# Performance work log

Measured on AMD Instinct MI355X. Metric: run time of the kernel, lower is better.

Reference implementation:

```python
import jax, jax.numpy as jnp
import numpy as np

B, S, T, H, E = 256, 512, 16, 1024, 512  # batch, src_len, trg_steps, hidden, emb_dim


def setup_inputs() -> dict:
    key = jax.random.key(0)
    ks = jax.random.split(key, 10)
    rn = lambda k, sh: jax.random.normal(k, sh, dtype=jnp.float32) * 0.05
    return {
        "trg_emb": rn(ks[0], (B, T, E)),
        "h0": rn(ks[1], (B, H)),
        "c0": rn(ks[2], (B, H)),
        "ctx": rn(ks[3], (B, S, H)),
        "src_len": jax.random.randint(ks[4], (B,), 1, S + 1, dtype=jnp.int32),
        "W_ih": rn(ks[5], (4 * H, E + H)),  # input-feeding: lstm in = emb + hidden
        "W_hh": rn(ks[6], (4 * H, H)),
        "b_ih": jnp.zeros((4 * H,), jnp.float32),
        "b_hh": jnp.zeros((4 * H,), jnp.float32),
        "W_in": rn(ks[7], (H, H)),    # attention linear_in (no bias)
        "W_out": rn(ks[8], (H, 2 * H)),  # attention linear_out (no bias)
    }


def reference(trg_emb, h0, c0, ctx, src_len, W_ih, W_hh, b_ih, b_hh, W_in, W_out):
    # mask[b, s] = s < src_len[b]
    mask = jnp.arange(S)[None, :] < src_len[:, None]  # (B, S)
    neg = jnp.float32(-1e9)

    def step(carry, emb_t):
        h, c, h_tilde = carry  # each (B, H); emb_t (B, E)
        # input feeding: concat target embedding with previous attentional vector
        x = jnp.concatenate([emb_t, h_tilde], axis=1)  # (B, E+H)
        gates = x @ W_ih.T + b_ih + h @ W_hh.T + b_hh  # (B, 4H), pytorch gate order i,f,g,o
        i, f, g, o = jnp.split(gates, 4, axis=1)
        i = jax.nn.sigmoid(i); f = jax.nn.sigmoid(f)
        g = jnp.tanh(g);       o = jax.nn.sigmoid(o)
        c = f * c + i * g
        h = o * jnp.tanh(c)
        # Luong soft-dot attention with src_len masking
        target = h @ W_in.T                                # (B, H)
        scores = jnp.einsum('bsh,bh->bs', ctx, target)     # (B, S)
        scores = jnp.where(mask, scores, neg)
        attn = jax.nn.softmax(scores, axis=-1)
        weighted = jnp.einsum('bs,bsh->bh', attn, ctx)     # (B, H)
        h_tilde = jnp.tanh(jnp.concatenate([weighted, h], axis=1) @ W_out.T)
        return (h, c, h_tilde), h_tilde

    # initial h_tilde = init_hidden[0] (per the original code)
    (h_f, c_f, _), hs = jax.lax.scan(step, (h0, c0, h0), jnp.swapaxes(trg_emb, 0, 1))
    output = jnp.swapaxes(hs, 0, 1)  # (B, T, H)
    return output, h_f, c_f
```

## Files before the change

kernel.cpp:

```cpp
#include <hip/hip_runtime.h>
#include <cstdint>
#include <cstddef>


#define B_ 256
#define S_ 512
#define T_ 16
#define H_ 1024
#define E_ 512
#define NBUF 6

typedef unsigned short u16;
using short8 = __attribute__((ext_vector_type(8))) short;
using f32x4  = __attribute__((ext_vector_type(4))) float;

__device__ __forceinline__ float bf2f(u16 u) {
  union { uint32_t i; float f; } v; v.i = ((uint32_t)u) << 16; return v.f;
}
__device__ __forceinline__ u16 f2bf(float f) {
  union { uint32_t i; float f; } v; v.f = f;
  uint32_t r = v.i + 0x7fffu + ((v.i >> 16) & 1u);
  return (u16)(r >> 16);
}
__device__ __forceinline__ ushort4 cvt4bf(float4 v) {
  ushort4 o; o.x = f2bf(v.x); o.y = f2bf(v.y); o.z = f2bf(v.z); o.w = f2bf(v.w);
  return o;
}
__device__ __forceinline__ float sigmoidf_(float x) { return 1.f / (1.f + __expf(-x)); }

__device__ __forceinline__ void gload_lds16(const void* g, void* l) {
  __builtin_amdgcn_global_load_lds(
      (const __attribute__((address_space(1))) void*)g,
      (__attribute__((address_space(3))) void*)l, 16, 0, 0);
}

struct Reg3 { const u16* A; int lda; const u16* B; int ldb; int kt; };

template <int EPI>
__global__ __launch_bounds__(256) void gemm_k(Reg3 r0, Reg3 r1, Reg3 r2,
                                              int nmb,
                                              float* __restrict__ Cf,
                                              u16* __restrict__ Cb,
                                              const float* __restrict__ bsum,
                                              float* __restrict__ cst,
                                              u16* __restrict__ hbfo,
                                              float* __restrict__ outHC,
                                              const int tstep) {
  __shared__ u16 smA[NBUF][4096];
  __shared__ u16 smB[NBUF][4096];
  const int tid = threadIdx.x;
  const int lane = tid & 63;
  const int wave = tid >> 6;
  const int wm = wave >> 1, wn = wave & 1;
  const int m0 = (blockIdx.x % nmb) * 64;
  const int n0 = (blockIdx.x / nmb) * 64;
  const int row16 = lane & 15;
  const int kg = lane >> 4;
  const int nt = r0.kt + r1.kt + r2.kt;

  auto stage = [&](int ti, int buf) {
    const int k01 = r0.kt + r1.kt;
    const u16* Ap = (ti < r0.kt) ? r0.A : (ti < k01) ? r1.A : r2.A;
    const u16* Bp = (ti < r0.kt) ? r0.B : (ti < k01) ? r1.B : r2.B;
    const int lda = (ti < r0.kt) ? r0.lda : (ti < k01) ? r1.lda : r2.lda;
    const int ldb = (ti < r0.kt) ? r0.ldb : (ti < k01) ? r1.ldb : r2.ldb;
    const int base = (ti < r0.kt) ? 0 : (ti < k01) ? r0.kt : k01;
    const int kr = (ti - base) << 6;
#pragma unroll
    for (int j = 0; j < 2; ++j) {
      const int c = j * 256 + tid;
      const int row = c >> 3, q = c & 7;
      gload_lds16(Ap + (size_t)(m0 + row) * lda + kr + ((q ^ (row & 7)) << 3),
                  (char*)&smA[buf][0] + (size_t)(j * 256 + wave * 64) * 16);
    }
#pragma unroll
    for (int j = 0; j < 2; ++j) {
      const int c = j * 256 + tid;
      const int row = c >> 3, q = c & 7;
      gload_lds16(Bp + (size_t)(n0 + row) * ldb + kr + ((q ^ (row & 7)) << 3),
                  (char*)&smB[buf][0] + (size_t)(j * 256 + wave * 64) * 16);
    }
  };

  f32x4 acc[2][2] = {};
  stage(0, 0);
  if (nt > 1) stage(1, 1);
  if (nt > 2) stage(2, 2);
  if (nt > 3) stage(3, 3);
  for (int ti = 0; ti < nt; ++ti) {
    const int buf = ti % NBUF;
    if (ti + 4 < nt) {
      stage(ti + 4, (ti + 4) % NBUF);
      asm volatile("s_waitcnt vmcnt(16)" ::: "memory");
    } else if (ti + 3 < nt) {
      asm volatile("s_waitcnt vmcnt(12)" ::: "memory");
    } else if (ti + 2 < nt) {
      asm volatile("s_waitcnt vmcnt(8)" ::: "memory");
    } else if (ti + 1 < nt) {
      asm volatile("s_waitcnt vmcnt(4)" ::: "memory");
    } else {
      asm volatile("s_waitcnt vmcnt(0)" ::: "memory");
    }
    __builtin_amdgcn_s_barrier();
    __builtin_amdgcn_sched_barrier(0);
#pragma unroll
    for (int ks = 0; ks < 2; ++ks) {
      short8 af[2], bfr[2];
#pragma unroll
      for (int mi = 0; mi < 2; ++mi) {
        const int R = wm * 32 + mi * 16 + row16;
        af[mi] = *(const short8*)((const char*)&smA[buf][0] +
                                  (size_t)(((R << 3) | ((ks * 4 + kg) ^ (R & 7))) << 4));
      }
#pragma unroll
      for (int ni = 0; ni < 2; ++ni) {
        const int R = wn * 32 + ni * 16 + row16;
        bfr[ni] = *(const short8*)((const char*)&smB[buf][0] +
                                   (size_t)(((R << 3) | ((ks * 4 + kg) ^ (R & 7))) << 4));
      }
      asm volatile("s_waitcnt lgkmcnt(0)" ::: "memory");
      __builtin_amdgcn_sched_barrier(0);
#pragma unroll
      for (int mi = 0; mi < 2; ++mi)
#pragma unroll
        for (int ni = 0; ni < 2; ++ni)
          acc[mi][ni] = __builtin_amdgcn_mfma_f32_16x16x32_bf16(af[mi], bfr[ni], acc[mi][ni], 0, 0, 0);
      __builtin_amdgcn_sched_barrier(0);
    }
  }
#pragma unroll
  for (int mi = 0; mi < 2; ++mi) {
#pragma unroll
    for (int ni = 0; ni < 2; ++ni) {
#pragma unroll
      for (int r = 0; r < 4; ++r) {
        const int row = m0 + wm * 32 + mi * 16 + (kg << 2) + r;
        const int col = n0 + wn * 32 + ni * 16 + row16;
        float v = acc[mi][ni][r];
        if (EPI == 1) {
          Cb[row * H_ + col] = f2bf(v);
        } else if (EPI == 2) {
          float tv = tanhf(v);
          Cf[(size_t)row * (T_ * H_) + (size_t)tstep * H_ + col] = tv;
          Cb[row * H_ + col] = f2bf(tv);
        } else {
          v += bsum[col];
          float v1 = __shfl_xor(v, 1);
          float v2 = __shfl_xor(v, 2);
          float v3 = __shfl_xor(v, 3);
          if ((lane & 3) == 0) {
            const int u = col >> 2;
            float iv = sigmoidf_(v);
            float fv = sigmoidf_(v1);
            float gv = tanhf(v2);
            float ov = sigmoidf_(v3);
            float cn = fv * cst[row * H_ + u] + iv * gv;
            float hn = ov * tanhf(cn);
            cst[row * H_ + u] = cn;
            hbfo[row * H_ + u] = f2bf(hn);
            if (outHC) {
              outHC[row * H_ + u] = hn;
              outHC[B_ * H_ + row * H_ + u] = cn;
            }
          }
        }
      }
    }
  }
}

__device__ __forceinline__ int fidx(int lane, int j) {
  return (j << 6) + ((lane + (j << 2)) & 63);
}

__global__ __launch_bounds__(512, 4) void attn_pair(const u16* __restrict__ tgt,
                                                    const u16* __restrict__ ctxc,
                                                    const int* __restrict__ woffs,
                                                    const int* __restrict__ src_len,
                                                    u16* __restrict__ wwbf,
                                                    float* __restrict__ pacc,
                                                    float* __restrict__ pml,
                                                    int* __restrict__ flag) {
  __shared__ float facc[7][1024];
  __shared__ float fm[8], fl[8];
  const int p = blockIdx.x >> 1;
  const int half = blockIdx.x & 1;
  const int tid = threadIdx.x;
  const int lane = tid & 63;
  const int wave = tid >> 6;
  const int len = src_len[p];
  const int len2 = (len + 1) >> 1;
  const u16* cb = ctxc + ((size_t)woffs[p] << 10);

  float tg[16];
  {
    const u16* tp = tgt + p * H_ + lane * 16;
    short8 v1 = *(const short8*)tp;
    short8 v2 = *(const short8*)(tp + 8);
#pragma unroll
    for (int j = 0; j < 8; ++j) { tg[j] = bf2f((u16)v1[j]); tg[8 + j] = bf2f((u16)v2[j]); }
  }
  float m = -1e30f, l = 0.f;
  float acc[16];
#pragma unroll
  for (int j = 0; j < 16; ++j) acc[j] = 0.f;

  auto process = [&](int s) {
    const u16* cr = cb + ((size_t)s << 10) + (lane << 4);
    short8 v1 = *(const short8*)cr;
    short8 v2 = *(const short8*)(cr + 8);
    float cf[16];
#pragma unroll
    for (int j = 0; j < 8; ++j) { cf[j] = bf2f((u16)v1[j]); cf[8 + j] = bf2f((u16)v2[j]); }
    float x = 0.f;
#pragma unroll
    for (int j = 0; j < 16; ++j) x += cf[j] * tg[j];
#pragma unroll
    for (int off = 1; off < 64; off <<= 1) x += __shfl_xor(x, off);
    if (x > m) {
      float sc_ = __expf(m - x);
      l *= sc_;
#pragma unroll
      for (int j = 0; j < 16; ++j) acc[j] *= sc_;
      m = x;
    }
    float pv = __expf(x - m);
    l += pv;
#pragma unroll
    for (int j = 0; j < 16; ++j) acc[j] += pv * cf[j];
  };

  const int lo = half ? len2 : 0;
  const int hi = half ? len : len2;
  for (int s = lo + wave; s < hi; s += 8) process(s);

  if (wave >= 1) {
#pragma unroll
    for (int j = 0; j < 16; ++j) facc[wave - 1][fidx(lane, j)] = acc[j];
    if (lane == 0) { fm[wave] = m; fl[wave] = l; }
  }
  __syncthreads();
  if (wave == 0) {
#pragma unroll
    for (int w = 1; w < 8; ++w) {
      float pm2 = fm[w], pl2 = fl[w];
      float M = fmaxf(m, pm2);
      float e1 = __expf(m - M), e2 = __expf(pm2 - M);
#pragma unroll
      for (int j = 0; j < 16; ++j)
        acc[j] = acc[j] * e1 + facc[w - 1][fidx(lane, j)] * e2;
      l = l * e1 + pl2 * e2;
      m = M;
    }
    if (half == 1) {
      float* pa = pacc + (size_t)p * 1024;
#pragma unroll
      for (int j4 = 0; j4 < 4; ++j4) {
        float4 v;
        v.x = acc[j4 * 4]; v.y = acc[j4 * 4 + 1];
        v.z = acc[j4 * 4 + 2]; v.w = acc[j4 * 4 + 3];
        *(float4*)&pa[lane * 16 + j4 * 4] = v;
      }
      if (lane == 0) { pml[2 * p] = m; pml[2 * p + 1] = l; }
      asm volatile("s_waitcnt vmcnt(0)" ::: "memory");
      if (lane == 0)
        __hip_atomic_store(flag + p, 1, __ATOMIC_RELEASE, __HIP_MEMORY_SCOPE_AGENT);
    } else {
      int got = 0;
      if (lane == 0) {
        for (unsigned c2 = 0; c2 < (1u << 10); ++c2) {
          if (__hip_atomic_load(flag + p, __ATOMIC_RELAXED, __HIP_MEMORY_SCOPE_AGENT) != 0) {
            got = 1; break;
          }
          __builtin_amdgcn_s_sleep(2);
        }
        if (got)
          (void)__hip_atomic_load(flag + p, __ATOMIC_ACQUIRE, __HIP_MEMORY_SCOPE_AGENT);
      }
      got = __shfl(got, 0);
      if (got) {
        const float* pa = pacc + (size_t)p * 1024;
        float pm2 = pml[2 * p], pl2 = pml[2 * p + 1];
        float M = fmaxf(m, pm2);
        float e1 = __expf(m - M), e2 = __expf(pm2 - M);
#pragma unroll
        for (int j = 0; j < 16; ++j)
          acc[j] = acc[j] * e1 + pa[lane * 16 + j] * e2;
        l = l * e1 + pl2 * e2;
        m = M;
      } else {
        for (int s = len2; s < len; ++s) process(s);
      }
      const float inv = 1.f / l;
#pragma unroll
      for (int j4 = 0; j4 < 4; ++j4) {
        ushort4 o;
        o.x = f2bf(acc[j4 * 4] * inv);
        o.y = f2bf(acc[j4 * 4 + 1] * inv);
        o.z = f2bf(acc[j4 * 4 + 2] * inv);
        o.w = f2bf(acc[j4 * 4 + 3] * inv);
        *(ushort4*)(wwbf + p * H_ + lane * 16 + j4 * 4) = o;
      }
    }
  }
}

__global__ __launch_bounds__(256) void convert_all(
    const float* __restrict__ W_ih, const float* __restrict__ W_hh,
    const float* __restrict__ W_in, const float* __restrict__ W_out,
    const float* __restrict__ trg_emb, const float* __restrict__ ctx,
    const float* __restrict__ b_ih, const float* __restrict__ b_hh,
    const float* __restrict__ h0, const float* __restrict__ c0,
    const int* __restrict__ src_len,
    u16* __restrict__ wWih, u16* __restrict__ wWhh, u16* __restrict__ wWin,
    u16* __restrict__ wWout, u16* __restrict__ wemb,
    float* __restrict__ wbsum, u16* __restrict__ wh0, u16* __restrict__ whtbf,
    float* __restrict__ wc, int* __restrict__ woffs, u16* __restrict__ ctxc) {
  __shared__ int tmp[256];
  const int bid = blockIdx.x;
  const int tid = threadIdx.x;
  const int gtid = bid * 256 + tid;
  const int GSZ = 1024 * 256;
  for (int i = gtid; i < 1572864; i += GSZ) {
    const int r = i / 384, c4 = i - r * 384;
    const int rp = ((r & 1023) << 2) + (r >> 10);
    ((ushort4*)wWih)[(size_t)rp * 384 + c4] = cvt4bf(((const float4*)W_ih)[i]);
  }
  for (int i = gtid; i < 1048576; i += GSZ) {
    const int r = i >> 8, c4 = i & 255;
    const int rp = ((r & 1023) << 2) + (r >> 10);
    ((ushort4*)wWhh)[(size_t)rp * 256 + c4] = cvt4bf(((const float4*)W_hh)[i]);
  }
  for (int i = gtid; i < 262144; i += GSZ)
    ((ushort4*)wWin)[i] = cvt4bf(((const float4*)W_in)[i]);
  for (int i = gtid; i < 524288; i += GSZ)
    ((ushort4*)wWout)[i] = cvt4bf(((const float4*)W_out)[i]);
  for (int i = gtid; i < 524288; i += GSZ)
    ((ushort4*)wemb)[i] = cvt4bf(((const float4*)trg_emb)[i]);
  if (gtid < 4096) {
    const int cp = ((gtid & 1023) << 2) + (gtid >> 10);
    wbsum[cp] = b_ih[gtid] + b_hh[gtid];
  }
  for (int i = gtid; i < 262144; i += GSZ) {
    u16 hb = f2bf(h0[i]);
    wh0[i] = hb;
    whtbf[i] = hb;
    wc[i] = c0[i];
  }
  if (bid >= 768) {
    const int b = bid - 768;
    tmp[tid] = (tid < b) ? src_len[tid] : 0;
    __syncthreads();
    for (int o = 128; o > 0; o >>= 1) {
      if (tid < o) tmp[tid] += tmp[tid + o];
      __syncthreads();
    }
    const int off = tmp[0];
    if (tid == 0) woffs[b] = off;
    const int n4 = src_len[b] << 8;
    const float4* s = (const float4*)(ctx + ((size_t)b << 19));
    ushort4* d = (ushort4*)(ctxc + ((size_t)off << 10));
    for (int i = tid; i < n4; i += 256) d[i] = cvt4bf(s[i]);
  }
}

extern "C" void kernel_launch(void* const* d_in, const int* in_sizes, int n_in,
                              void* d_out, int out_size, void* d_ws, size_t ws_size,
                              hipStream_t stream) {
  const float* trg_emb = (const float*)d_in[0];
  const float* h0      = (const float*)d_in[1];
  const float* c0      = (const float*)d_in[2];
  const float* ctx     = (const float*)d_in[3];
  const int*   src_len = (const int*)d_in[4];
  const float* W_ih    = (const float*)d_in[5];
  const float* W_hh    = (const float*)d_in[6];
  const float* b_ih    = (const float*)d_in[7];
  const float* b_hh    = (const float*)d_in[8];
  const float* W_in    = (const float*)d_in[9];
  const float* W_out   = (const float*)d_in[10];
  float* out = (float*)d_out;

  char* w = (char*)d_ws;
  size_t off = 0;
  auto alloc = [&](size_t bytes) { char* p = w + off; off += bytes; return p; };
  u16*   wWih  = (u16*)  alloc(12582912);
  u16*   wWhh  = (u16*)  alloc(8388608);
  u16*   wWin  = (u16*)  alloc(2097152);
  u16*   wWout = (u16*)  alloc(4194304);
  u16*   wemb  = (u16*)  alloc(4194304);
  float* wbsum = (float*)alloc(16384);
  float* wc    = (float*)alloc(1048576);
  u16*   wh0   = (u16*)  alloc(524288);
  u16*   wh1   = (u16*)  alloc(524288);
  u16*   whtbf = (u16*)  alloc(524288);
  u16*   wtgt  = (u16*)  alloc(524288);
  u16*   wwbf  = (u16*)  alloc(524288);
  int*   woffs = (int*)  alloc(1024);
  int*   wflag = (int*)  alloc(16384);
  float* pacc  = (float*)alloc(1048576);
  float* pml   = (float*)alloc(2048);
  u16*   wctxc = (u16*)  alloc(268435456);
  (void)ws_size;

  hipMemsetAsync(wflag, 0, 16384, stream);
  convert_all<<<dim3(1024), dim3(256), 0, stream>>>(
      W_ih, W_hh, W_in, W_out, trg_emb, ctx, b_ih, b_hh, h0, c0, src_len,
      wWih, wWhh, wWin, wWout, wemb, wbsum, wh0, whtbf, wc, woffs, wctxc);

  Reg3 rz = { nullptr, 0, nullptr, 0, 0 };
  for (int t = 0; t < T_; ++t) {
    const u16* hcur = (t & 1) ? wh1 : wh0;
    u16* hnxt = (t & 1) ? wh0 : wh1;
    Reg3 g0 = { wemb + (size_t)t * E_, T_ * E_, wWih,      E_ + H_, 8 };
    Reg3 g1 = { whtbf,                 H_,      wWih + E_, E_ + H_, 16 };
    Reg3 g2 = { hcur,                  H_,      wWhh,      H_,      16 };
    gemm_k<3><<<dim3(256), dim3(256), 0, stream>>>(
        g0, g1, g2, 4, nullptr, nullptr, wbsum, wc, hnxt,
        (t == T_ - 1) ? out + (size_t)B_ * T_ * H_ : nullptr, 0);
    Reg3 i0 = { hnxt, H_, wWin, H_, 16 };
    gemm_k<1><<<dim3(64), dim3(256), 0, stream>>>(
        i0, rz, rz, 4, nullptr, wtgt, nullptr, nullptr, nullptr, nullptr, 0);
    attn_pair<<<dim3(512), dim3(512), 0, stream>>>(
        wtgt, wctxc, woffs, src_len, wwbf, pacc, pml, wflag + t * 256);
    Reg3 o0 = { wwbf, H_, wWout,      2 * H_, 16 };
    Reg3 o1 = { hnxt, H_, wWout + H_, 2 * H_, 16 };
    gemm_k<2><<<dim3(64), dim3(256), 0, stream>>>(
        o0, o1, rz, 4, out, whtbf, nullptr, nullptr, nullptr, nullptr, t);
  }
}
```

Measured before the change: 1.914 ms.

## Fuse attention linear_in GEMM into attention kernel with flag-based handoff and length ordering

```diff
diff --git a/kernel.cpp b/kernel.cpp
--- a/kernel.cpp
+++ b/kernel.cpp
@@ -32,6 +32,10 @@
   __builtin_amdgcn_global_load_lds(
       (const __attribute__((address_space(1))) void*)g,
       (__attribute__((address_space(3))) void*)l, 16, 0, 0);
+}
+
+__device__ __forceinline__ void st_flag(int* p) {
+  __hip_atomic_store(p, 1, __ATOMIC_RELEASE, __HIP_MEMORY_SCOPE_AGENT);
 }
 
 struct Reg3 { const u16* A; int lda; const u16* B; int ldb; int kt; };
@@ -137,9 +141,7 @@
         const int row = m0 + wm * 32 + mi * 16 + (kg << 2) + r;
         const int col = n0 + wn * 32 + ni * 16 + row16;
         float v = acc[mi][ni][r];
-        if (EPI == 1) {
-          Cb[row * H_ + col] = f2bf(v);
-        } else if (EPI == 2) {
+        if (EPI == 2) {
           float tv = tanhf(v);
           Cf[(size_t)row * (T_ * H_) + (size_t)tstep * H_ + col] = tv;
           Cb[row * H_ + col] = f2bf(tv);
@@ -173,33 +175,165 @@
   return (j << 6) + ((lane + (j << 2)) & 63);
 }
 
-__global__ __launch_bounds__(512, 4) void attn_pair(const u16* __restrict__ tgt,
-                                                    const u16* __restrict__ ctxc,
-                                                    const int* __restrict__ woffs,
-                                                    const int* __restrict__ src_len,
-                                                    u16* __restrict__ wwbf,
-                                                    float* __restrict__ pacc,
-                                                    float* __restrict__ pml,
-                                                    int* __restrict__ flag) {
-  __shared__ float facc[7][1024];
-  __shared__ float fm[8], fl[8];
-  const int p = blockIdx.x >> 1;
-  const int half = blockIdx.x & 1;
+struct AP {
+  const u16* hrow;
+  const u16* Win;
+  u16* tgt;
+  const u16* ctxc;
+  const int* woffs;
+  const int* src_len;
+  const int* worder;
+  u16* wwbf;
+  float* pacc;
+  float* pml;
+  int* tflag;
+  int* pflag;
+};
+
+union SMemF {
+  struct { u16 A[4][4096]; u16 B[4][4096]; } g;
+  struct { float facc[7][1024]; float fm[8]; float fl[8];
+           float tgtf[1024]; int ok; } a;
+};
+
+__global__ __launch_bounds__(512, 4) void attn_fused(AP P) {
+  __shared__ SMemF sm;
   const int tid = threadIdx.x;
+  const int bid = blockIdx.x;
   const int lane = tid & 63;
   const int wave = tid >> 6;
-  const int len = src_len[p];
+
+  if (bid < 64) {
+    const int m0 = (bid & 3) * 64;
+    const int n0 = (bid >> 2) * 64;
+    if (tid < 256) {
+      const int wv = tid >> 6;
+      const int wm = wv >> 1, wn = wv & 1;
+      const int row16 = lane & 15, kg = lane >> 4;
+      auto stage = [&](int ti, int buf) {
+        const int kr = ti << 6;
+#pragma unroll
+        for (int j = 0; j < 2; ++j) {
+          const int c = j * 256 + tid;
+          const int r = c >> 3, q = c & 7;
+          gload_lds16(P.hrow + (size_t)(m0 + r) * H_ + kr + ((q ^ (r & 7)) << 3),
+                      (char*)&sm.g.A[buf][0] + (size_t)(j * 256 + wv * 64) * 16);
+        }
+#pragma unroll
+        for (int j = 0; j < 2; ++j) {
+          const int c = j * 256 + tid;
+          const int r = c >> 3, q = c & 7;
+          gload_lds16(P.Win + (size_t)(n0 + r) * H_ + kr + ((q ^ (r & 7)) << 3),
+                      (char*)&sm.g.B[buf][0] + (size_t)(j * 256 + wv * 64) * 16);
+        }
+      };
+      f32x4 acc[2][2] = {};
+      stage(0, 0);
+      stage(1, 1);
+      for (int ti = 0; ti < 16; ++ti) {
+        const int buf = ti & 3;
+        if (ti + 2 < 16) {
+          stage(ti + 2, (ti + 2) & 3);
+          asm volatile("s_waitcnt vmcnt(8)" ::: "memory");
+        } else if (ti + 1 < 16) {
+          asm volatile("s_waitcnt vmcnt(4)" ::: "memory");
+        } else {
+          asm volatile("s_waitcnt vmcnt(0)" ::: "memory");
+        }
+        __builtin_amdgcn_s_barrier();
+        __builtin_amdgcn_sched_barrier(0);
+#pragma unroll
+        for (int ks = 0; ks < 2; ++ks) {
+          short8 af[2], bfr[2];
+#pragma unroll
+          for (int mi = 0; mi < 2; ++mi) {
+            const int R = wm * 32 + mi * 16 + row16;
+            af[mi] = *(const short8*)((const char*)&sm.g.A[buf][0] +
+                                      (size_t)(((R << 3) | ((ks * 4 + kg) ^ (R & 7))) << 4));
+          }
+#pragma unroll
+          for (int ni = 0; ni < 2; ++ni) {
+            const int R = wn * 32 + ni * 16 + row16;
+            bfr[ni] = *(const short8*)((const char*)&sm.g.B[buf][0] +
+                                       (size_t)(((R << 3) | ((ks * 4 + kg) ^ (R & 7))) << 4));
+          }
+          asm volatile("s_waitcnt lgkmcnt(0)" ::: "memory");
+          __builtin_amdgcn_sched_barrier(0);
+#pragma unroll
+          for (int mi = 0; mi < 2; ++mi)
+#pragma unroll
+            for (int ni = 0; ni < 2; ++ni)
+              acc[mi][ni] = __builtin_amdgcn_mfma_f32_16x16x32_bf16(af[mi], bfr[ni], acc[mi][ni], 0, 0, 0);
+          __builtin_amdgcn_sched_barrier(0);
+        }
+      }
+#pragma unroll
+      for (int mi = 0; mi < 2; ++mi)
+#pragma unroll
+        for (int ni = 0; ni < 2; ++ni)
+#pragma unroll
+          for (int r = 0; r < 4; ++r) {
+            const int row = m0 + wm * 32 + mi * 16 + (kg << 2) + r;
+            const int col = n0 + wn * 32 + ni * 16 + row16;
+            P.tgt[row * H_ + col] = f2bf(acc[mi][ni][r]);
+          }
+    } else {
+      for (int i = 0; i < 16; ++i) __builtin_amdgcn_s_barrier();
+    }
+    __syncthreads();
+    if (tid == 0) st_flag(P.tflag + (bid & 3) * 16 + (bid >> 2));
+  }
+
+  const int p = bid >> 1;
+  const int half = bid & 1;
+  const int row = P.worder[p];
+  const int len = P.src_len[row];
   const int len2 = (len + 1) >> 1;
-  const u16* cb = ctxc + ((size_t)woffs[p] << 10);
+  const u16* cb = P.ctxc + ((size_t)P.woffs[row] << 10);
+  const int mt = row >> 6;
+
+  {
+    int got = 1;
+    if (wave == 0) {
+      if (lane < 16) {
+        int* tf = P.tflag + mt * 16 + lane;
+        unsigned c = 0;
+        while (__hip_atomic_load(tf, __ATOMIC_RELAXED, __HIP_MEMORY_SCOPE_AGENT) == 0 &&
+               c < (1u << 16)) {
+          __builtin_amdgcn_s_sleep(4);
+          ++c;
+        }
+        got = (__hip_atomic_load(tf, __ATOMIC_ACQUIRE, __HIP_MEMORY_SCOPE_AGENT) != 0) ? 1 : 0;
+      }
+      unsigned long long mk = __ballot(got != 0);
+      if (lane == 0) sm.a.ok = ((mk & 0xFFFFull) == 0xFFFFull) ? 1 : 0;
+    }
+    __syncthreads();
+  }
+  const int allok = sm.a.ok;
+  if (!allok) {
+    const u16* hr = P.hrow + (size_t)row * H_;
+    for (int j = tid; j < H_; j += 512) {
+      float a = 0.f;
+      const u16* wr = P.Win + (size_t)j * H_;
+      for (int k = 0; k < H_; ++k) a += bf2f(hr[k]) * bf2f(wr[k]);
+      sm.a.tgtf[j] = bf2f(f2bf(a));
+    }
+    __syncthreads();
+  }
 
   float tg[16];
-  {
-    const u16* tp = tgt + p * H_ + lane * 16;
+  if (allok) {
+    const u16* tp = P.tgt + row * H_ + lane * 16;
     short8 v1 = *(const short8*)tp;
     short8 v2 = *(const short8*)(tp + 8);
 #pragma unroll
     for (int j = 0; j < 8; ++j) { tg[j] = bf2f((u16)v1[j]); tg[8 + j] = bf2f((u16)v2[j]); }
-  }
+  } else {
+#pragma unroll
+    for (int j = 0; j < 16; ++j) tg[j] = sm.a.tgtf[lane * 16 + j];
+  }
+
   float m = -1e30f, l = 0.f;
   float acc[16];
 #pragma unroll
@@ -234,26 +368,27 @@
   const int hi = half ? len : len2;
   for (int s = lo + wave; s < hi; s += 8) process(s);
 
+  __syncthreads();
   if (wave >= 1) {
 #pragma unroll
-    for (int j = 0; j < 16; ++j) facc[wave - 1][fidx(lane, j)] = acc[j];
-    if (lane == 0) { fm[wave] = m; fl[wave] = l; }
+    for (int j = 0; j < 16; ++j) sm.a.facc[wave - 1][fidx(lane, j)] = acc[j];
+    if (lane == 0) { sm.a.fm[wave] = m; sm.a.fl[wave] = l; }
   }
   __syncthreads();
   if (wave == 0) {
 #pragma unroll
     for (int w = 1; w < 8; ++w) {
-      float pm2 = fm[w], pl2 = fl[w];
+      float pm2 = sm.a.fm[w], pl2 = sm.a.fl[w];
       float M = fmaxf(m, pm2);
       float e1 = __expf(m - M), e2 = __expf(pm2 - M);
 #pragma unroll
       for (int j = 0; j < 16; ++j)
-        acc[j] = acc[j] * e1 + facc[w - 1][fidx(lane, j)] * e2;
+        acc[j] = acc[j] * e1 + sm.a.facc[w - 1][fidx(lane, j)] * e2;
       l = l * e1 + pl2 * e2;
       m = M;
     }
     if (half == 1) {
-      float* pa = pacc + (size_t)p * 1024;
+      float* pa = P.pacc + (size_t)p * 1024;
 #pragma unroll
       for (int j4 = 0; j4 < 4; ++j4) {
         float4 v;
@@ -261,26 +396,25 @@
         v.z = acc[j4 * 4 + 2]; v.w = acc[j4 * 4 + 3];
         *(float4*)&pa[lane * 16 + j4 * 4] = v;
       }
-      if (lane == 0) { pml[2 * p] = m; pml[2 * p + 1] = l; }
+      if (lane == 0) { P.pml[2 * p] = m; P.pml[2 * p + 1] = l; }
       asm volatile("s_waitcnt vmcnt(0)" ::: "memory");
-      if (lane == 0)
-        __hip_atomic_store(flag + p, 1, __ATOMIC_RELEASE, __HIP_MEMORY_SCOPE_AGENT);
+      if (lane == 0) st_flag(P.pflag + p);
     } else {
       int got = 0;
       if (lane == 0) {
         for (unsigned c2 = 0; c2 < (1u << 10); ++c2) {
-          if (__hip_atomic_load(flag + p, __ATOMIC_RELAXED, __HIP_MEMORY_SCOPE_AGENT) != 0) {
+          if (__hip_atomic_load(P.pflag + p, __ATOMIC_RELAXED, __HIP_MEMORY_SCOPE_AGENT) != 0) {
             got = 1; break;
           }
           __builtin_amdgcn_s_sleep(2);
         }
         if (got)
-          (void)__hip_atomic_load(flag + p, __ATOMIC_ACQUIRE, __HIP_MEMORY_SCOPE_AGENT);
+          (void)__hip_atomic_load(P.pflag + p, __ATOMIC_ACQUIRE, __HIP_MEMORY_SCOPE_AGENT);
       }
       got = __shfl(got, 0);
       if (got) {
-        const float* pa = pacc + (size_t)p * 1024;
-        float pm2 = pml[2 * p], pl2 = pml[2 * p + 1];
+        const float* pa = P.pacc + (size_t)p * 1024;
+        float pm2 = P.pml[2 * p], pl2 = P.pml[2 * p + 1];
         float M = fmaxf(m, pm2);
         float e1 = __expf(m - M), e2 = __expf(pm2 - M);
 #pragma unroll
@@ -299,7 +433,7 @@
         o.y = f2bf(acc[j4 * 4 + 1] * inv);
         o.z = f2bf(acc[j4 * 4 + 2] * inv);
         o.w = f2bf(acc[j4 * 4 + 3] * inv);
-        *(ushort4*)(wwbf + p * H_ + lane * 16 + j4 * 4) = o;
+        *(ushort4*)(P.wwbf + row * H_ + lane * 16 + j4 * 4) = o;
       }
     }
   }
@@ -315,8 +449,10 @@
     u16* __restrict__ wWih, u16* __restrict__ wWhh, u16* __restrict__ wWin,
     u16* __restrict__ wWout, u16* __restrict__ wemb,
     float* __restrict__ wbsum, u16* __restrict__ wh0, u16* __restrict__ whtbf,
-    float* __restrict__ wc, int* __restrict__ woffs, u16* __restrict__ ctxc) {
+    float* __restrict__ wc, int* __restrict__ woffs, u16* __restrict__ ctxc,
+    int* __restrict__ worder) {
   __shared__ int tmp[256];
+  __shared__ int skey[256];
   const int bid = blockIdx.x;
   const int tid = threadIdx.x;
   const int gtid = bid * 256 + tid;
@@ -361,6 +497,22 @@
     const float4* s = (const float4*)(ctx + ((size_t)b << 19));
     ushort4* d = (ushort4*)(ctxc + ((size_t)off << 10));
     for (int i = tid; i < n4; i += 256) d[i] = cvt4bf(s[i]);
+  }
+  if (bid == 0) {
+    skey[tid] = (src_len[tid] << 16) | tid;
+    __syncthreads();
+    for (int k = 2; k <= 256; k <<= 1) {
+      for (int j = k >> 1; j > 0; j >>= 1) {
+        const int ixj = tid ^ j;
+        if (ixj > tid) {
+          int a = skey[tid], b = skey[ixj];
+          bool asc = ((tid & k) == 0);
+          if ((a > b) == asc) { skey[tid] = b; skey[ixj] = a; }
+        }
+        __syncthreads();
+      }
+    }
+    worder[tid] = (tid < 32 ? skey[tid] : skey[287 - tid]) & 0xFFFF;
   }
 }
 
@@ -383,29 +535,32 @@
   char* w = (char*)d_ws;
   size_t off = 0;
   auto alloc = [&](size_t bytes) { char* p = w + off; off += bytes; return p; };
-  u16*   wWih  = (u16*)  alloc(12582912);
-  u16*   wWhh  = (u16*)  alloc(8388608);
-  u16*   wWin  = (u16*)  alloc(2097152);
-  u16*   wWout = (u16*)  alloc(4194304);
-  u16*   wemb  = (u16*)  alloc(4194304);
-  float* wbsum = (float*)alloc(16384);
-  float* wc    = (float*)alloc(1048576);
-  u16*   wh0   = (u16*)  alloc(524288);
-  u16*   wh1   = (u16*)  alloc(524288);
-  u16*   whtbf = (u16*)  alloc(524288);
-  u16*   wtgt  = (u16*)  alloc(524288);
-  u16*   wwbf  = (u16*)  alloc(524288);
-  int*   woffs = (int*)  alloc(1024);
-  int*   wflag = (int*)  alloc(16384);
-  float* pacc  = (float*)alloc(1048576);
-  float* pml   = (float*)alloc(2048);
-  u16*   wctxc = (u16*)  alloc(268435456);
+  u16*   wWih   = (u16*)  alloc(12582912);
+  u16*   wWhh   = (u16*)  alloc(8388608);
+  u16*   wWin   = (u16*)  alloc(2097152);
+  u16*   wWout  = (u16*)  alloc(4194304);
+  u16*   wemb   = (u16*)  alloc(4194304);
+  float* wbsum  = (float*)alloc(16384);
+  float* wc     = (float*)alloc(1048576);
+  u16*   wh0    = (u16*)  alloc(524288);
+  u16*   wh1    = (u16*)  alloc(524288);
+  u16*   whtbf  = (u16*)  alloc(524288);
+  u16*   wwbf   = (u16*)  alloc(524288);
+  int*   woffs  = (int*)  alloc(1024);
+  int*   worder = (int*)  alloc(1024);
+  int*   flags  = (int*)  alloc(20480);
+  u16*   wtgt16 = (u16*)  alloc(8388608);
+  float* pacc16 = (float*)alloc(16777216);
+  float* pml16  = (float*)alloc(32768);
+  u16*   wctxc  = (u16*)  alloc(268435456);
   (void)ws_size;
-
-  hipMemsetAsync(wflag, 0, 16384, stream);
+  int* tflags = flags;
+  int* pflags = flags + 16 * 64;
+
+  hipMemsetAsync(flags, 0, 20480, stream);
   convert_all<<<dim3(1024), dim3(256), 0, stream>>>(
       W_ih, W_hh, W_in, W_out, trg_emb, ctx, b_ih, b_hh, h0, c0, src_len,
-      wWih, wWhh, wWin, wWout, wemb, wbsum, wh0, whtbf, wc, woffs, wctxc);
+      wWih, wWhh, wWin, wWout, wemb, wbsum, wh0, whtbf, wc, woffs, wctxc, worder);
 
   Reg3 rz = { nullptr, 0, nullptr, 0, 0 };
   for (int t = 0; t < T_; ++t) {
@@ -417,11 +572,16 @@
     gemm_k<3><<<dim3(256), dim3(256), 0, stream>>>(
         g0, g1, g2, 4, nullptr, nullptr, wbsum, wc, hnxt,
         (t == T_ - 1) ? out + (size_t)B_ * T_ * H_ : nullptr, 0);
-    Reg3 i0 = { hnxt, H_, wWin, H_, 16 };
-    gemm_k<1><<<dim3(64), dim3(256), 0, stream>>>(
-        i0, rz, rz, 4, nullptr, wtgt, nullptr, nullptr, nullptr, nullptr, 0);
-    attn_pair<<<dim3(512), dim3(512), 0, stream>>>(
-        wtgt, wctxc, woffs, src_len, wwbf, pacc, pml, wflag + t * 256);
+    AP ap;
+    ap.hrow = hnxt; ap.Win = wWin;
+    ap.tgt = wtgt16 + (size_t)t * 262144;
+    ap.ctxc = wctxc; ap.woffs = woffs; ap.src_len = src_len; ap.worder = worder;
+    ap.wwbf = wwbf;
+    ap.pacc = pacc16 + (size_t)t * 262144;
+    ap.pml = pml16 + t * 512;
+    ap.tflag = tflags + t * 64;
+    ap.pflag = pflags + t * 256;
+    attn_fused<<<dim3(512), dim3(512), 0, stream>>>(ap);
     Reg3 o0 = { wwbf, H_, wWout,      2 * H_, 16 };
     Reg3 o1 = { hnxt, H_, wWout + H_, 2 * H_, 16 };
     gemm_k<2><<<dim3(64), dim3(256), 0, stream>>>(
```

Measured after the change: 2.023 ms. 1.06x slower.
